# Kernel tuning notes

Measured on AMD Instinct MI355X. Metric: run time of the kernel, lower is better.

The kernel has to match this reference:

```python
import jax, jax.numpy as jnp
import numpy as np

N_CLASSES = 16
N_CATEGORY = 4096
OUT = 512
BS = 4096


def setup_inputs() -> dict:
    key = jax.random.key(0)
    k1, k2, k3 = jax.random.split(key, 3)
    batch = jax.random.normal(k1, (BS, N_CATEGORY), dtype=jnp.float32)
    classes = jax.random.randint(k2, (BS,), 0, N_CLASSES, dtype=jnp.int32)
    # Stacked per-class Linear weights, each [out, in] like nn.Linear.weight.
    W = jax.random.normal(k3, (N_CLASSES, OUT, N_CATEGORY), dtype=jnp.float32) * 0.02
    return {"batch": batch, "classes": classes, "W": W}


def reference(batch, classes, W):
    # Original: result[i] = W[classes[i]] @ batch[i]  (per-sample class-indexed linear).
    # Vectorized: compute all experts' outputs [b, c, o], then select per-sample class.
    all_out = jnp.einsum('bi,coi->bco', batch, W)
    out = jnp.take_along_axis(all_out, classes.astype(jnp.int32)[:, None, None], axis=1)
    return out[:, 0, :]  # [bs, out]
```

## Files before the change

### kernel.cpp

```cpp
#include <hip/hip_runtime.h>
#include <hip/hip_bf16.h>

typedef __attribute__((ext_vector_type(4))) float f32x4;
typedef __attribute__((ext_vector_type(8))) short s16x8;

#define NCLS 16
#define NCAT 4096
#define NOUT 512
#define NBS  4096

#define BM 128
#define BN 128
#define BK 32
#define NSPLIT 4
#define KSPLIT (NCAT / NSPLIT)
#define NIT    (KSPLIT / BK)
#define MAXTILES 48

#define WS_NT    0
#define WS_CBASE 1
#define WS_TCLS  32
#define WS_TM0   96
#define WS_SIDX  160

__global__ __launch_bounds__(256) void prep_kernel(const int* __restrict__ cls,
                                                   int* __restrict__ ws) {
  __shared__ int lcnt[NCLS * 256];
  __shared__ int cb[NCLS];
  const int t = threadIdx.x;

  int cl[16];
  #pragma unroll
  for (int j = 0; j < 16; ++j) cl[j] = cls[j * 256 + t];

  int cnt[NCLS];
  #pragma unroll
  for (int c = 0; c < NCLS; ++c) cnt[c] = 0;
  #pragma unroll
  for (int j = 0; j < 16; ++j) {
    #pragma unroll
    for (int c = 0; c < NCLS; ++c) cnt[c] += (cl[j] == c) ? 1 : 0;
  }
  #pragma unroll
  for (int c = 0; c < NCLS; ++c) lcnt[c * 256 + t] = cnt[c];
  __syncthreads();

  for (int d = 1; d < 256; d <<= 1) {
    int add[NCLS];
    #pragma unroll
    for (int c = 0; c < NCLS; ++c) add[c] = (t >= d) ? lcnt[c * 256 + t - d] : 0;
    __syncthreads();
    #pragma unroll
    for (int c = 0; c < NCLS; ++c) if (t >= d) lcnt[c * 256 + t] += add[c];
    __syncthreads();
  }

  if (t == 0) {
    int acc = 0, ntt = 0;
    for (int c = 0; c < NCLS; ++c) {
      cb[c] = acc;
      ws[WS_CBASE + c] = acc;
      int tot = lcnt[c * 256 + 255];
      for (int m0 = 0; m0 < tot; m0 += BM) {
        ws[WS_TCLS + ntt] = c;
        ws[WS_TM0 + ntt] = m0;
        ++ntt;
      }
      acc += tot;
    }
    ws[WS_CBASE + NCLS] = acc;
    ws[WS_NT] = ntt;
  }
  __syncthreads();

  #pragma unroll
  for (int j = 0; j < 16; ++j) {
    int c = cl[j];
    int within = 0;
    #pragma unroll
    for (int j2 = 0; j2 < 16; ++j2) within += (j2 < j && cl[j2] == c) ? 1 : 0;
    ws[WS_SIDX + cb[c] + (lcnt[c * 256 + t] - cnt[c]) + within] = j * 256 + t;
  }
}

typedef const __attribute__((address_space(1))) void* gas_ptr;
typedef __attribute__((address_space(3))) void* las_ptr;

__device__ __forceinline__ void gl_lds16(const void* g, void* l) {
  __builtin_amdgcn_global_load_lds((gas_ptr)g, (las_ptr)l, 16, 0, 0);
}

__device__ __forceinline__ void pk2(float x0, float x1, unsigned& hb, unsigned& lb) {
  __hip_bfloat162 h2 = __float22bfloat162_rn(make_float2(x0, x1));
  float2 hf = __bfloat1622float2(h2);
  __hip_bfloat162 l2 = __float22bfloat162_rn(make_float2(x0 - hf.x, x1 - hf.y));
  __builtin_memcpy(&hb, &h2, 4);
  __builtin_memcpy(&lb, &l2, 4);
}

__device__ __forceinline__ void cvt8(f32x4 p, f32x4 q, s16x8& hi, s16x8& lo) {
  union { s16x8 v; unsigned u[4]; } H, L;
  pk2(p[0], p[1], H.u[0], L.u[0]);
  pk2(p[2], p[3], H.u[1], L.u[1]);
  pk2(q[0], q[1], H.u[2], L.u[2]);
  pk2(q[2], q[3], H.u[3], L.u[3]);
  hi = H.v; lo = L.v;
}

__global__ __launch_bounds__(256, 2) void gemm_kernel(const float* __restrict__ batch,
                                                      const float* __restrict__ W,
                                                      const int* __restrict__ ws,
                                                      float* __restrict__ out) {
  const int tile = blockIdx.x;
  if (tile >= ws[WS_NT]) return;
  const int c    = ws[WS_TCLS + tile];
  const int m0   = ws[WS_TM0 + tile];
  const int base = ws[WS_CBASE + c];
  const int Mc   = ws[WS_CBASE + c + 1] - base;
  const int n0   = blockIdx.y * BN;
  const int k0   = blockIdx.z * KSPLIT;
  const int* sidx = ws + WS_SIDX + base;

  __shared__ char lds[65536];

  const int t    = threadIdx.x;
  const int lane = t & 63;
  const int wv   = t >> 6;
  const int l15  = lane & 15;

  const int rsub = lane >> 3;
  const int ko   = (((lane & 7) ^ rsub) << 4);
  const char* aga[4];
  const char* bga[4];
  #pragma unroll
  for (int j = 0; j < 4; ++j) {
    const int rr = 32 * wv + 8 * j + rsub;
    const int ar = sidx[min(m0 + rr, Mc - 1)];
    aga[j] = (const char*)batch + ((size_t)ar * NCAT + k0) * 4 + ko;
    const int br = c * NOUT + n0 + rr;
    bga[j] = (const char*)W + ((size_t)br * NCAT + k0) * 4 + ko;
  }

  char* const stA = lds + (32 * wv) * 128;

  const int wm  = (wv >> 1) * 64;
  const int wn  = (wv & 1) * 64;
  const int kb0 = (lane >> 4) * 32;

  f32x4 acc[4][4];
  #pragma unroll
  for (int i = 0; i < 4; ++i)
    #pragma unroll
    for (int j = 0; j < 4; ++j) acc[i][j] = (f32x4){0.f, 0.f, 0.f, 0.f};

  #pragma unroll
  for (int j = 0; j < 4; ++j) {
    gl_lds16(aga[j] + 0 * 128, stA + j * 1024);
    gl_lds16(bga[j] + 0 * 128, stA + 16384 + j * 1024);
  }
  #pragma unroll
  for (int j = 0; j < 4; ++j) {
    gl_lds16(aga[j] + 1 * 128, stA + 32768 + j * 1024);
    gl_lds16(bga[j] + 1 * 128, stA + 32768 + 16384 + j * 1024);
  }

  for (int it = 0; it < NIT; ++it) {
    if (it < NIT - 1) asm volatile("s_waitcnt vmcnt(8)" ::: "memory");
    else              asm volatile("s_waitcnt vmcnt(0)" ::: "memory");
    __builtin_amdgcn_s_barrier();
    asm volatile("" ::: "memory");

    {
      const char* const bufp = lds + (it & 1) * 32768;
      s16x8 Ah[4], Al[4], Bh[4], Bl[4];
      #pragma unroll
      for (int i = 0; i < 4; ++i) {
        const int m = wm + i * 16 + l15;
        const char* rowp = bufp + m * 128;
        const int swzm = (m & 7) << 4;
        f32x4 p = *(const f32x4*)(rowp + ((kb0) ^ swzm));
        f32x4 q = *(const f32x4*)(rowp + ((kb0 + 16) ^ swzm));
        cvt8(p, q, Ah[i], Al[i]);
        const int n = wn + i * 16 + l15;
        const char* rowq = bufp + 16384 + n * 128;
        const int swzn = (n & 7) << 4;
        f32x4 r = *(const f32x4*)(rowq + ((kb0) ^ swzn));
        f32x4 s = *(const f32x4*)(rowq + ((kb0 + 16) ^ swzn));
        cvt8(r, s, Bh[i], Bl[i]);
      }
      #pragma unroll
      for (int i = 0; i < 4; ++i)
        #pragma unroll
        for (int j = 0; j < 4; ++j) {
          acc[i][j] = __builtin_amdgcn_mfma_f32_16x16x32_bf16(Ah[i], Bh[j], acc[i][j], 0, 0, 0);
          acc[i][j] = __builtin_amdgcn_mfma_f32_16x16x32_bf16(Ah[i], Bl[j], acc[i][j], 0, 0, 0);
          acc[i][j] = __builtin_amdgcn_mfma_f32_16x16x32_bf16(Al[i], Bh[j], acc[i][j], 0, 0, 0);
        }
    }

    asm volatile("" ::: "memory");
    __builtin_amdgcn_s_barrier();
    if (it + 2 < NIT) {
      char* const dst = lds + (it & 1) * 32768 + (32 * wv) * 128;
      const int koff = (it + 2) * 128;
      #pragma unroll
      for (int j = 0; j < 4; ++j) {
        gl_lds16(aga[j] + koff, dst + j * 1024);
        gl_lds16(bga[j] + koff, dst + 16384 + j * 1024);
      }
    }
  }

  const int r4 = (lane >> 4) * 4;
  #pragma unroll
  for (int i = 0; i < 4; ++i) {
    #pragma unroll
    for (int jj = 0; jj < 4; ++jj) {
      const int mloc = wm + i * 16 + r4 + jj;
      const int gm = m0 + mloc;
      if (gm < Mc) {
        const int sample = sidx[gm];
        float* orow = out + (size_t)sample * NOUT + n0 + wn;
        #pragma unroll
        for (int j = 0; j < 4; ++j) {
          atomicAdd(orow + j * 16 + l15, acc[i][j][jj]);
        }
      }
    }
  }
}

extern "C" void kernel_launch(void* const* d_in, const int* in_sizes, int n_in,
                              void* d_out, int out_size, void* d_ws, size_t ws_size,
                              hipStream_t stream) {
  const float* batch = (const float*)d_in[0];
  const int*   cls   = (const int*)d_in[1];
  const float* W     = (const float*)d_in[2];
  float* out = (float*)d_out;
  int*   ws  = (int*)d_ws;

  prep_kernel<<<1, 256, 0, stream>>>(cls, ws);
  hipMemsetAsync(d_out, 0, (size_t)out_size * sizeof(float), stream);
  gemm_kernel<<<dim3(MAXTILES, NOUT / BN, NSPLIT), 256, 0, stream>>>(batch, W, ws, out);
}
```

Baseline: 314.5 us.

## Halve N tile to 64 and restructure double-buffered pipeline for 3 blocks/CU

```diff
diff --git a/kernel.cpp b/kernel.cpp
--- a/kernel.cpp
+++ b/kernel.cpp
@@ -10,12 +10,13 @@
 #define NBS  4096
 
 #define BM 128
-#define BN 128
+#define BN 64
 #define BK 32
 #define NSPLIT 4
 #define KSPLIT (NCAT / NSPLIT)
 #define NIT    (KSPLIT / BK)
 #define MAXTILES 48
+#define BUFSZ  24576
 
 #define WS_NT    0
 #define WS_CBASE 1
@@ -107,7 +108,7 @@
   hi = H.v; lo = L.v;
 }
 
-__global__ __launch_bounds__(256, 2) void gemm_kernel(const float* __restrict__ batch,
+__global__ __launch_bounds__(256, 3) void gemm_kernel(const float* __restrict__ batch,
                                                       const float* __restrict__ W,
                                                       const int* __restrict__ ws,
                                                       float* __restrict__ out) {
@@ -121,7 +122,7 @@
   const int k0   = blockIdx.z * KSPLIT;
   const int* sidx = ws + WS_SIDX + base;
 
-  __shared__ char lds[65536];
+  __shared__ char lds[2 * BUFSZ];
 
   const int t    = threadIdx.x;
   const int lane = t & 63;
@@ -129,87 +130,83 @@
   const int l15  = lane & 15;
 
   const int rsub = lane >> 3;
-  const int ko   = (((lane & 7) ^ rsub) << 4);
+  const int cswz = (((lane & 7) ^ rsub) << 4);
   const char* aga[4];
-  const char* bga[4];
   #pragma unroll
   for (int j = 0; j < 4; ++j) {
     const int rr = 32 * wv + 8 * j + rsub;
     const int ar = sidx[min(m0 + rr, Mc - 1)];
-    aga[j] = (const char*)batch + ((size_t)ar * NCAT + k0) * 4 + ko;
-    const int br = c * NOUT + n0 + rr;
-    bga[j] = (const char*)W + ((size_t)br * NCAT + k0) * 4 + ko;
-  }
-
-  char* const stA = lds + (32 * wv) * 128;
+    aga[j] = (const char*)batch + ((size_t)ar * NCAT + k0) * 4 + cswz;
+  }
+  const char* bga[2];
+  #pragma unroll
+  for (int j = 0; j < 2; ++j) {
+    const int br = c * NOUT + n0 + 16 * wv + 8 * j + rsub;
+    bga[j] = (const char*)W + ((size_t)br * NCAT + k0) * 4 + cswz;
+  }
 
   const int wm  = (wv >> 1) * 64;
-  const int wn  = (wv & 1) * 64;
+  const int wn  = (wv & 1) * 32;
   const int kb0 = (lane >> 4) * 32;
-
-  f32x4 acc[4][4];
+  const int swz = (l15 & 7) << 4;
+
+  f32x4 acc[4][2];
   #pragma unroll
   for (int i = 0; i < 4; ++i)
     #pragma unroll
-    for (int j = 0; j < 4; ++j) acc[i][j] = (f32x4){0.f, 0.f, 0.f, 0.f};
-
-  #pragma unroll
-  for (int j = 0; j < 4; ++j) {
-    gl_lds16(aga[j] + 0 * 128, stA + j * 1024);
-    gl_lds16(bga[j] + 0 * 128, stA + 16384 + j * 1024);
-  }
-  #pragma unroll
-  for (int j = 0; j < 4; ++j) {
-    gl_lds16(aga[j] + 1 * 128, stA + 32768 + j * 1024);
-    gl_lds16(bga[j] + 1 * 128, stA + 32768 + 16384 + j * 1024);
-  }
-
+    for (int j = 0; j < 2; ++j) acc[i][j] = (f32x4){0.f, 0.f, 0.f, 0.f};
+
+  #define STAGE(bufofs, kbyte)                                                  \
+    do {                                                                        \
+      _Pragma("unroll")                                                         \
+      for (int j = 0; j < 4; ++j)                                               \
+        gl_lds16(aga[j] + (kbyte), lds + (bufofs) + (32 * wv + 8 * j) * 128);   \
+      _Pragma("unroll")                                                         \
+      for (int j = 0; j < 2; ++j)                                               \
+        gl_lds16(bga[j] + (kbyte), lds + (bufofs) + 16384 + (16 * wv + 8 * j) * 128); \
+    } while (0)
+
+  STAGE(0, 0);
+  asm volatile("s_waitcnt vmcnt(0)" ::: "memory");
+  __builtin_amdgcn_s_barrier();
+  asm volatile("" ::: "memory");
+
+  int cur = 0;
   for (int it = 0; it < NIT; ++it) {
-    if (it < NIT - 1) asm volatile("s_waitcnt vmcnt(8)" ::: "memory");
-    else              asm volatile("s_waitcnt vmcnt(0)" ::: "memory");
+    if (it + 1 < NIT) STAGE((cur ^ 1) * BUFSZ, (it + 1) * 128);
+
+    const char* const bufp = lds + cur * BUFSZ;
+    s16x8 Ah[4], Al[4], Bh[2], Bl[2];
+    #pragma unroll
+    for (int i = 0; i < 4; ++i) {
+      const char* rowp = bufp + (wm + i * 16 + l15) * 128;
+      f32x4 p = *(const f32x4*)(rowp + (kb0 ^ swz));
+      f32x4 q = *(const f32x4*)(rowp + ((kb0 + 16) ^ swz));
+      cvt8(p, q, Ah[i], Al[i]);
+    }
+    #pragma unroll
+    for (int j = 0; j < 2; ++j) {
+      const char* rowq = bufp + 16384 + (wn + j * 16 + l15) * 128;
+      f32x4 r = *(const f32x4*)(rowq + (kb0 ^ swz));
+      f32x4 s = *(const f32x4*)(rowq + ((kb0 + 16) ^ swz));
+      cvt8(r, s, Bh[j], Bl[j]);
+    }
+    #pragma unroll
+    for (int i = 0; i < 4; ++i)
+      #pragma unroll
+      for (int j = 0; j < 2; ++j) {
+        acc[i][j] = __builtin_amdgcn_mfma_f32_16x16x32_bf16(Ah[i], Bh[j], acc[i][j], 0, 0, 0);
+        acc[i][j] = __builtin_amdgcn_mfma_f32_16x16x32_bf16(Ah[i], Bl[j], acc[i][j], 0, 0, 0);
+        acc[i][j] = __builtin_amdgcn_mfma_f32_16x16x32_bf16(Al[i], Bh[j], acc[i][j], 0, 0, 0);
+      }
+
+    __builtin_amdgcn_sched_barrier(0);
+    asm volatile("s_waitcnt vmcnt(0)" ::: "memory");
     __builtin_amdgcn_s_barrier();
     asm volatile("" ::: "memory");
-
-    {
-      const char* const bufp = lds + (it & 1) * 32768;
-      s16x8 Ah[4], Al[4], Bh[4], Bl[4];
-      #pragma unroll
-      for (int i = 0; i < 4; ++i) {
-        const int m = wm + i * 16 + l15;
-        const char* rowp = bufp + m * 128;
-        const int swzm = (m & 7) << 4;
-        f32x4 p = *(const f32x4*)(rowp + ((kb0) ^ swzm));
-        f32x4 q = *(const f32x4*)(rowp + ((kb0 + 16) ^ swzm));
-        cvt8(p, q, Ah[i], Al[i]);
-        const int n = wn + i * 16 + l15;
-        const char* rowq = bufp + 16384 + n * 128;
-        const int swzn = (n & 7) << 4;
-        f32x4 r = *(const f32x4*)(rowq + ((kb0) ^ swzn));
-        f32x4 s = *(const f32x4*)(rowq + ((kb0 + 16) ^ swzn));
-        cvt8(r, s, Bh[i], Bl[i]);
-      }
-      #pragma unroll
-      for (int i = 0; i < 4; ++i)
-        #pragma unroll
-        for (int j = 0; j < 4; ++j) {
-          acc[i][j] = __builtin_amdgcn_mfma_f32_16x16x32_bf16(Ah[i], Bh[j], acc[i][j], 0, 0, 0);
-          acc[i][j] = __builtin_amdgcn_mfma_f32_16x16x32_bf16(Ah[i], Bl[j], acc[i][j], 0, 0, 0);
-          acc[i][j] = __builtin_amdgcn_mfma_f32_16x16x32_bf16(Al[i], Bh[j], acc[i][j], 0, 0, 0);
-        }
-    }
-
-    asm volatile("" ::: "memory");
-    __builtin_amdgcn_s_barrier();
-    if (it + 2 < NIT) {
-      char* const dst = lds + (it & 1) * 32768 + (32 * wv) * 128;
-      const int koff = (it + 2) * 128;
-      #pragma unroll
-      for (int j = 0; j < 4; ++j) {
-        gl_lds16(aga[j] + koff, dst + j * 1024);
-        gl_lds16(bga[j] + koff, dst + 16384 + j * 1024);
-      }
-    }
-  }
+    cur ^= 1;
+  }
+  #undef STAGE
 
   const int r4 = (lane >> 4) * 4;
   #pragma unroll
@@ -222,7 +219,7 @@
         const int sample = sidx[gm];
         float* orow = out + (size_t)sample * NOUT + n0 + wn;
         #pragma unroll
-        for (int j = 0; j < 4; ++j) {
+        for (int j = 0; j < 2; ++j) {
           atomicAdd(orow + j * 16 + l15, acc[i][j][jj]);
         }
       }
```

Measured after the change: 311.5 us. About the same (-1.0%).

## Convert fp32 to split bf16 once per tile when staging through registers into LDS

Applied to the files above, without the earlier changes.

```diff
diff --git a/kernel.cpp b/kernel.cpp
--- a/kernel.cpp
+++ b/kernel.cpp
@@ -12,10 +12,12 @@
 #define BM 128
 #define BN 128
 #define BK 32
-#define NSPLIT 4
+#define NSPLIT 8
 #define KSPLIT (NCAT / NSPLIT)
 #define NIT    (KSPLIT / BK)
 #define MAXTILES 48
+#define ABYTES 16384
+#define BUFSZ  32768
 
 #define WS_NT    0
 #define WS_CBASE 1
@@ -83,13 +85,6 @@
   }
 }
 
-typedef const __attribute__((address_space(1))) void* gas_ptr;
-typedef __attribute__((address_space(3))) void* las_ptr;
-
-__device__ __forceinline__ void gl_lds16(const void* g, void* l) {
-  __builtin_amdgcn_global_load_lds((gas_ptr)g, (las_ptr)l, 16, 0, 0);
-}
-
 __device__ __forceinline__ void pk2(float x0, float x1, unsigned& hb, unsigned& lb) {
   __hip_bfloat162 h2 = __float22bfloat162_rn(make_float2(x0, x1));
   float2 hf = __bfloat1622float2(h2);
@@ -98,13 +93,17 @@
   __builtin_memcpy(&lb, &l2, 4);
 }
 
-__device__ __forceinline__ void cvt8(f32x4 p, f32x4 q, s16x8& hi, s16x8& lo) {
-  union { s16x8 v; unsigned u[4]; } H, L;
-  pk2(p[0], p[1], H.u[0], L.u[0]);
-  pk2(p[2], p[3], H.u[1], L.u[1]);
-  pk2(q[0], q[1], H.u[2], L.u[2]);
-  pk2(q[2], q[3], H.u[3], L.u[3]);
-  hi = H.v; lo = L.v;
+__device__ __forceinline__ void cvt16(const f32x4* r, uint4* H, uint4* L) {
+  #pragma unroll
+  for (int j = 0; j < 4; ++j) {
+    unsigned h0, l0, h1, l1;
+    pk2(r[j][0], r[j][1], h0, l0);
+    pk2(r[j][2], r[j][3], h1, l1);
+    ((unsigned*)H)[2 * j]     = h0;
+    ((unsigned*)H)[2 * j + 1] = h1;
+    ((unsigned*)L)[2 * j]     = l0;
+    ((unsigned*)L)[2 * j + 1] = l1;
+  }
 }
 
 __global__ __launch_bounds__(256, 2) void gemm_kernel(const float* __restrict__ batch,
@@ -121,31 +120,54 @@
   const int k0   = blockIdx.z * KSPLIT;
   const int* sidx = ws + WS_SIDX + base;
 
-  __shared__ char lds[65536];
+  __shared__ char lds[2 * BUFSZ];
 
   const int t    = threadIdx.x;
   const int lane = t & 63;
   const int wv   = t >> 6;
   const int l15  = lane & 15;
 
-  const int rsub = lane >> 3;
-  const int ko   = (((lane & 7) ^ rsub) << 4);
-  const char* aga[4];
-  const char* bga[4];
-  #pragma unroll
-  for (int j = 0; j < 4; ++j) {
-    const int rr = 32 * wv + 8 * j + rsub;
-    const int ar = sidx[min(m0 + rr, Mc - 1)];
-    aga[j] = (const char*)batch + ((size_t)ar * NCAT + k0) * 4 + ko;
-    const int br = c * NOUT + n0 + rr;
-    bga[j] = (const char*)W + ((size_t)br * NCAT + k0) * 4 + ko;
-  }
-
-  char* const stA = lds + (32 * wv) * 128;
-
-  const int wm  = (wv >> 1) * 64;
-  const int wn  = (wv & 1) * 64;
-  const int kb0 = (lane >> 4) * 32;
+  const int r = t >> 1;
+  const int h = t & 1;
+  const int swzw = (r & 7) << 4;
+  const int ar = sidx[min(m0 + r, Mc - 1)];
+  const char* abase = (const char*)(batch + (size_t)ar * NCAT + k0) + h * 64;
+  const char* bbase = (const char*)(W + ((size_t)c * NOUT + n0 + r) * NCAT + k0) + h * 64;
+
+  const int wm   = (wv >> 1) * 64;
+  const int wn   = (wv & 1) * 64;
+  const int kg16 = (lane >> 4) * 16;
+  const int srd  = (l15 & 7) << 4;
+
+  f32x4 ra[4], rb[4];
+
+  #define LOADR(IT)                                                \
+    do {                                                           \
+      const char* ap_ = abase + (IT) * 128;                        \
+      const char* bp_ = bbase + (IT) * 128;                        \
+      _Pragma("unroll")                                            \
+      for (int j_ = 0; j_ < 4; ++j_) {                             \
+        ra[j_] = *(const f32x4*)(ap_ + j_ * 16);                   \
+        rb[j_] = *(const f32x4*)(bp_ + j_ * 16);                   \
+      }                                                            \
+    } while (0)
+
+  #define CVTWRITE(bo)                                                          \
+    do {                                                                        \
+      uint4 H_[2], L_[2];                                                       \
+      cvt16(ra, H_, L_);                                                        \
+      char* d_ = lds + (bo) + r * 128;                                          \
+      *(uint4*)(d_ + ((h * 32) ^ swzw))        = H_[0];                         \
+      *(uint4*)(d_ + ((h * 32 + 16) ^ swzw))   = H_[1];                         \
+      *(uint4*)(d_ + ((64 + h * 32) ^ swzw))      = L_[0];                      \
+      *(uint4*)(d_ + ((64 + h * 32 + 16) ^ swzw)) = L_[1];                      \
+      cvt16(rb, H_, L_);                                                        \
+      char* e_ = lds + (bo) + ABYTES + r * 128;                                 \
+      *(uint4*)(e_ + ((h * 32) ^ swzw))        = H_[0];                         \
+      *(uint4*)(e_ + ((h * 32 + 16) ^ swzw))   = H_[1];                         \
+      *(uint4*)(e_ + ((64 + h * 32) ^ swzw))      = L_[0];                      \
+      *(uint4*)(e_ + ((64 + h * 32 + 16) ^ swzw)) = L_[1];                      \
+    } while (0)
 
   f32x4 acc[4][4];
   #pragma unroll
@@ -153,63 +175,47 @@
     #pragma unroll
     for (int j = 0; j < 4; ++j) acc[i][j] = (f32x4){0.f, 0.f, 0.f, 0.f};
 
-  #pragma unroll
-  for (int j = 0; j < 4; ++j) {
-    gl_lds16(aga[j] + 0 * 128, stA + j * 1024);
-    gl_lds16(bga[j] + 0 * 128, stA + 16384 + j * 1024);
-  }
-  #pragma unroll
-  for (int j = 0; j < 4; ++j) {
-    gl_lds16(aga[j] + 1 * 128, stA + 32768 + j * 1024);
-    gl_lds16(bga[j] + 1 * 128, stA + 32768 + 16384 + j * 1024);
-  }
+  LOADR(0);
+  CVTWRITE(0);
+  LOADR(1);
+  asm volatile("s_waitcnt lgkmcnt(0)" ::: "memory");
+  __builtin_amdgcn_s_barrier();
+  asm volatile("" ::: "memory");
 
   for (int it = 0; it < NIT; ++it) {
-    if (it < NIT - 1) asm volatile("s_waitcnt vmcnt(8)" ::: "memory");
-    else              asm volatile("s_waitcnt vmcnt(0)" ::: "memory");
+    const int cur = it & 1;
+    if (it + 1 < NIT) CVTWRITE((cur ^ 1) * BUFSZ);
+    if (it + 2 < NIT) LOADR(it + 2);
+
+    const char* const bufA = lds + cur * BUFSZ;
+    const char* const bufB = bufA + ABYTES;
+    s16x8 Ah[4], Al[4], Bh[4], Bl[4];
+    #pragma unroll
+    for (int i = 0; i < 4; ++i) {
+      const char* rp = bufA + (wm + i * 16 + l15) * 128;
+      Ah[i] = *(const s16x8*)(rp + (kg16 ^ srd));
+      Al[i] = *(const s16x8*)(rp + ((64 + kg16) ^ srd));
+      const char* rq = bufB + (wn + i * 16 + l15) * 128;
+      Bh[i] = *(const s16x8*)(rq + (kg16 ^ srd));
+      Bl[i] = *(const s16x8*)(rq + ((64 + kg16) ^ srd));
+    }
+    __builtin_amdgcn_s_setprio(1);
+    #pragma unroll
+    for (int i = 0; i < 4; ++i)
+      #pragma unroll
+      for (int j = 0; j < 4; ++j) {
+        acc[i][j] = __builtin_amdgcn_mfma_f32_16x16x32_bf16(Ah[i], Bh[j], acc[i][j], 0, 0, 0);
+        acc[i][j] = __builtin_amdgcn_mfma_f32_16x16x32_bf16(Ah[i], Bl[j], acc[i][j], 0, 0, 0);
+        acc[i][j] = __builtin_amdgcn_mfma_f32_16x16x32_bf16(Al[i], Bh[j], acc[i][j], 0, 0, 0);
+      }
+    __builtin_amdgcn_s_setprio(0);
+
+    asm volatile("s_waitcnt lgkmcnt(0)" ::: "memory");
     __builtin_amdgcn_s_barrier();
     asm volatile("" ::: "memory");
-
-    {
-      const char* const bufp = lds + (it & 1) * 32768;
-      s16x8 Ah[4], Al[4], Bh[4], Bl[4];
-      #pragma unroll
-      for (int i = 0; i < 4; ++i) {
-        const int m = wm + i * 16 + l15;
-        const char* rowp = bufp + m * 128;
-        const int swzm = (m & 7) << 4;
-        f32x4 p = *(const f32x4*)(rowp + ((kb0) ^ swzm));
-        f32x4 q = *(const f32x4*)(rowp + ((kb0 + 16) ^ swzm));
-        cvt8(p, q, Ah[i], Al[i]);
-        const int n = wn + i * 16 + l15;
-        const char* rowq = bufp + 16384 + n * 128;
-        const int swzn = (n & 7) << 4;
-        f32x4 r = *(const f32x4*)(rowq + ((kb0) ^ swzn));
-        f32x4 s = *(const f32x4*)(rowq + ((kb0 + 16) ^ swzn));
-        cvt8(r, s, Bh[i], Bl[i]);
-      }
-      #pragma unroll
-      for (int i = 0; i < 4; ++i)
-        #pragma unroll
-        for (int j = 0; j < 4; ++j) {
-          acc[i][j] = __builtin_amdgcn_mfma_f32_16x16x32_bf16(Ah[i], Bh[j], acc[i][j], 0, 0, 0);
-          acc[i][j] = __builtin_amdgcn_mfma_f32_16x16x32_bf16(Ah[i], Bl[j], acc[i][j], 0, 0, 0);
-          acc[i][j] = __builtin_amdgcn_mfma_f32_16x16x32_bf16(Al[i], Bh[j], acc[i][j], 0, 0, 0);
-        }
-    }
-
-    asm volatile("" ::: "memory");
-    __builtin_amdgcn_s_barrier();
-    if (it + 2 < NIT) {
-      char* const dst = lds + (it & 1) * 32768 + (32 * wv) * 128;
-      const int koff = (it + 2) * 128;
-      #pragma unroll
-      for (int j = 0; j < 4; ++j) {
-        gl_lds16(aga[j] + koff, dst + j * 1024);
-        gl_lds16(bga[j] + koff, dst + 16384 + j * 1024);
-      }
-    }
-  }
+  }
+  #undef LOADR
+  #undef CVTWRITE
 
   const int r4 = (lane >> 4) * 4;
   #pragma unroll
```

Result: no change. 318.1 us (+1.1%).

## Single-buffer LDS, double split-K, raise occupancy with setprio around MFMA

Applied to the files above, without the earlier changes.

```diff
diff --git a/kernel.cpp b/kernel.cpp
--- a/kernel.cpp
+++ b/kernel.cpp
@@ -12,7 +12,7 @@
 #define BM 128
 #define BN 128
 #define BK 32
-#define NSPLIT 4
+#define NSPLIT 8
 #define KSPLIT (NCAT / NSPLIT)
 #define NIT    (KSPLIT / BK)
 #define MAXTILES 48
@@ -107,7 +107,7 @@
   hi = H.v; lo = L.v;
 }
 
-__global__ __launch_bounds__(256, 2) void gemm_kernel(const float* __restrict__ batch,
+__global__ __launch_bounds__(256, 5) void gemm_kernel(const float* __restrict__ batch,
                                                       const float* __restrict__ W,
                                                       const int* __restrict__ ws,
                                                       float* __restrict__ out) {
@@ -121,7 +121,9 @@
   const int k0   = blockIdx.z * KSPLIT;
   const int* sidx = ws + WS_SIDX + base;
 
-  __shared__ char lds[65536];
+  __shared__ char lds[32768];
+  char* const ldsA = lds;
+  char* const ldsB = lds + 16384;
 
   const int t    = threadIdx.x;
   const int lane = t & 63;
@@ -129,19 +131,17 @@
   const int l15  = lane & 15;
 
   const int rsub = lane >> 3;
-  const int ko   = (((lane & 7) ^ rsub) << 4);
+  const int cswz = (((lane & 7) ^ rsub) << 4);
   const char* aga[4];
   const char* bga[4];
   #pragma unroll
   for (int j = 0; j < 4; ++j) {
     const int rr = 32 * wv + 8 * j + rsub;
     const int ar = sidx[min(m0 + rr, Mc - 1)];
-    aga[j] = (const char*)batch + ((size_t)ar * NCAT + k0) * 4 + ko;
+    aga[j] = (const char*)batch + ((size_t)ar * NCAT + k0) * 4 + cswz;
     const int br = c * NOUT + n0 + rr;
-    bga[j] = (const char*)W + ((size_t)br * NCAT + k0) * 4 + ko;
-  }
-
-  char* const stA = lds + (32 * wv) * 128;
+    bga[j] = (const char*)W + ((size_t)br * NCAT + k0) * 4 + cswz;
+  }
 
   const int wm  = (wv >> 1) * 64;
   const int wn  = (wv & 1) * 64;
@@ -153,62 +153,48 @@
     #pragma unroll
     for (int j = 0; j < 4; ++j) acc[i][j] = (f32x4){0.f, 0.f, 0.f, 0.f};
 
-  #pragma unroll
-  for (int j = 0; j < 4; ++j) {
-    gl_lds16(aga[j] + 0 * 128, stA + j * 1024);
-    gl_lds16(bga[j] + 0 * 128, stA + 16384 + j * 1024);
-  }
-  #pragma unroll
-  for (int j = 0; j < 4; ++j) {
-    gl_lds16(aga[j] + 1 * 128, stA + 32768 + j * 1024);
-    gl_lds16(bga[j] + 1 * 128, stA + 32768 + 16384 + j * 1024);
-  }
-
   for (int it = 0; it < NIT; ++it) {
-    if (it < NIT - 1) asm volatile("s_waitcnt vmcnt(8)" ::: "memory");
-    else              asm volatile("s_waitcnt vmcnt(0)" ::: "memory");
     __builtin_amdgcn_s_barrier();
     asm volatile("" ::: "memory");
 
-    {
-      const char* const bufp = lds + (it & 1) * 32768;
-      s16x8 Ah[4], Al[4], Bh[4], Bl[4];
-      #pragma unroll
-      for (int i = 0; i < 4; ++i) {
-        const int m = wm + i * 16 + l15;
-        const char* rowp = bufp + m * 128;
-        const int swzm = (m & 7) << 4;
-        f32x4 p = *(const f32x4*)(rowp + ((kb0) ^ swzm));
-        f32x4 q = *(const f32x4*)(rowp + ((kb0 + 16) ^ swzm));
-        cvt8(p, q, Ah[i], Al[i]);
-        const int n = wn + i * 16 + l15;
-        const char* rowq = bufp + 16384 + n * 128;
-        const int swzn = (n & 7) << 4;
-        f32x4 r = *(const f32x4*)(rowq + ((kb0) ^ swzn));
-        f32x4 s = *(const f32x4*)(rowq + ((kb0 + 16) ^ swzn));
-        cvt8(r, s, Bh[i], Bl[i]);
-      }
-      #pragma unroll
-      for (int i = 0; i < 4; ++i)
-        #pragma unroll
-        for (int j = 0; j < 4; ++j) {
-          acc[i][j] = __builtin_amdgcn_mfma_f32_16x16x32_bf16(Ah[i], Bh[j], acc[i][j], 0, 0, 0);
-          acc[i][j] = __builtin_amdgcn_mfma_f32_16x16x32_bf16(Ah[i], Bl[j], acc[i][j], 0, 0, 0);
-          acc[i][j] = __builtin_amdgcn_mfma_f32_16x16x32_bf16(Al[i], Bh[j], acc[i][j], 0, 0, 0);
-        }
+    const int kbyte = it * 128;
+    #pragma unroll
+    for (int j = 0; j < 4; ++j)
+      gl_lds16(aga[j] + kbyte, ldsA + (32 * wv + 8 * j) * 128);
+    #pragma unroll
+    for (int j = 0; j < 4; ++j)
+      gl_lds16(bga[j] + kbyte, ldsB + (32 * wv + 8 * j) * 128);
+
+    asm volatile("s_waitcnt vmcnt(0)" ::: "memory");
+    __builtin_amdgcn_s_barrier();
+    asm volatile("" ::: "memory");
+
+    s16x8 Ah[4], Al[4], Bh[4], Bl[4];
+    #pragma unroll
+    for (int i = 0; i < 4; ++i) {
+      const int m = wm + i * 16 + l15;
+      const char* rowp = ldsA + m * 128;
+      const int swzm = (m & 7) << 4;
+      f32x4 p = *(const f32x4*)(rowp + (kb0 ^ swzm));
+      f32x4 q = *(const f32x4*)(rowp + ((kb0 + 16) ^ swzm));
+      cvt8(p, q, Ah[i], Al[i]);
+      const int n = wn + i * 16 + l15;
+      const char* rowq = ldsB + n * 128;
+      const int swzn = (n & 7) << 4;
+      f32x4 rr = *(const f32x4*)(rowq + (kb0 ^ swzn));
+      f32x4 ss = *(const f32x4*)(rowq + ((kb0 + 16) ^ swzn));
+      cvt8(rr, ss, Bh[i], Bl[i]);
     }
-
-    asm volatile("" ::: "memory");
-    __builtin_amdgcn_s_barrier();
-    if (it + 2 < NIT) {
-      char* const dst = lds + (it & 1) * 32768 + (32 * wv) * 128;
-      const int koff = (it + 2) * 128;
+    __builtin_amdgcn_s_setprio(1);
+    #pragma unroll
+    for (int i = 0; i < 4; ++i)
       #pragma unroll
       for (int j = 0; j < 4; ++j) {
-        gl_lds16(aga[j] + koff, dst + j * 1024);
-        gl_lds16(bga[j] + koff, dst + 16384 + j * 1024);
+        acc[i][j] = __builtin_amdgcn_mfma_f32_16x16x32_bf16(Ah[i], Bh[j], acc[i][j], 0, 0, 0);
+        acc[i][j] = __builtin_amdgcn_mfma_f32_16x16x32_bf16(Ah[i], Bl[j], acc[i][j], 0, 0, 0);
+        acc[i][j] = __builtin_amdgcn_mfma_f32_16x16x32_bf16(Al[i], Bh[j], acc[i][j], 0, 0, 0);
       }
-    }
+    __builtin_amdgcn_s_setprio(0);
   }
 
   const int r4 = (lane >> 4) * 4;
```

Measured after the change: 817.0 us. 160% more time.
